# Performance work log

Hardware: AMD Instinct MI355X
Metric: run time of the kernel (lower is better)

Reference implementation:

```python
import jax, jax.numpy as jnp
import numpy as np

V, D, H, T, S = 50000, 256, 512, 16, 8192
H2 = H // 2
START, END = 0, 1
NEG = -10000.0


def setup_inputs() -> dict:
    key = jax.random.key(0)
    ks = jax.random.split(key, 16)

    def rn(k, shape, scale=0.1):
        return jax.random.normal(k, shape, dtype=jnp.float32) * scale

    sentence = jax.random.randint(ks[0], (S,), 0, V)
    emb = rn(ks[1], (V, D), 1.0)
    w_ih_f = rn(ks[2], (4 * H2, D)); w_hh_f = rn(ks[3], (4 * H2, H2))
    b_f = rn(ks[4], (4 * H2,))  # b_ih + b_hh fused
    w_ih_b = rn(ks[5], (4 * H2, D)); w_hh_b = rn(ks[6], (4 * H2, H2))
    b_b = rn(ks[7], (4 * H2,))
    h0_f = rn(ks[8], (H2,), 1.0); c0_f = rn(ks[9], (H2,), 1.0)
    h0_b = rn(ks[10], (H2,), 1.0); c0_b = rn(ks[11], (H2,), 1.0)
    w_out = rn(ks[12], (T, H)); b_out = rn(ks[13], (T,))
    trans = jax.random.normal(ks[14], (T, T), dtype=jnp.float32)
    # transition[START, :] = -10000 ; transition[:, END] = -10000
    trans = trans.at[START, :].set(NEG).at[:, END].set(NEG)
    return {"sentence": sentence, "emb": emb,
            "w_ih_f": w_ih_f, "w_hh_f": w_hh_f, "b_f": b_f,
            "w_ih_b": w_ih_b, "w_hh_b": w_hh_b, "b_b": b_b,
            "h0_f": h0_f, "c0_f": c0_f, "h0_b": h0_b, "c0_b": c0_b,
            "w_out": w_out, "b_out": b_out, "trans": trans}


def _lstm(pre, w_hh, h0, c0):
    # pre: [S, 4*H2] precomputed input projections (x @ W_ih^T + b)
    def step(carry, pre_t):
        h, c = carry
        g = pre_t + w_hh @ h
        i, f, gg, o = jnp.split(g, 4)  # torch gate order: i, f, g, o
        i = jax.nn.sigmoid(i); f = jax.nn.sigmoid(f)
        gg = jnp.tanh(gg); o = jax.nn.sigmoid(o)
        c = f * c + i * gg
        h = o * jnp.tanh(c)
        return (h, c), h
    _, hs = jax.lax.scan(step, (h0, c0), pre)
    return hs  # [S, H2]


def reference(sentence, emb, w_ih_f, w_hh_f, b_f, w_ih_b, w_hh_b, b_b,
              h0_f, c0_f, h0_b, c0_b, w_out, b_out, trans):
    x = emb[sentence]                               # [S, D]
    pre_f = x @ w_ih_f.T + b_f                      # [S, 4*H2]
    pre_b = x[::-1] @ w_ih_b.T + b_b                # reverse direction
    hs_f = _lstm(pre_f, w_hh_f, h0_f, c0_f)         # [S, H2]
    hs_b = _lstm(pre_b, w_hh_b, h0_b, c0_b)[::-1]   # [S, H2]
    feats = jnp.concatenate([hs_f, hs_b], axis=-1) @ w_out.T + b_out  # [S, T]

    # Viterbi (max-plus DP), vectorized over the tag dimension.
    init = jnp.full((T,), NEG, dtype=feats.dtype).at[START].set(0.0)

    def vit_step(score, emit_t):
        cand = score[None, :] + trans               # [T_next, T_prev]
        best = jnp.argmax(cand, axis=1)             # backpointers [T]
        score = jnp.max(cand, axis=1) + emit_t
        return score, best

    last, back = jax.lax.scan(vit_step, init, feats)  # back: [S, T] int
    final = last + trans[END]                       # [T]
    best_last = jnp.argmax(final)
    path_score = final[best_last]

    # Backtrack: path[S-1] = best_last, path[t-1] = back[t][path[t]]
    def back_step(tag, bp_t):
        return bp_t[tag], tag
    _, path = jax.lax.scan(back_step, best_last, back, reverse=True)
    return path_score, path
```

## Files before the change

### kernel.cpp

```cpp
#include <hip/hip_runtime.h>
#include <math.h>

#define SLEN 8192
#define DIM  256
#define H2N  256
#define G4   1024
#define NTAG 16
#define NEGV (-10000.0f)

#define OFF_PRE_F   0
#define OFF_PRE_B   (SLEN*G4)
#define OFF_HS_F    (2*SLEN*G4)
#define OFF_HS_B    (2*SLEN*G4 + SLEN*H2N)
#define OFF_FEATS   (2*SLEN*G4 + 2*SLEN*H2N)
#define OFF_MBOX    (OFF_FEATS + SLEN*NTAG)
#define WS_NEEDED   ((size_t)(OFF_MBOX + 1024) * 4)

typedef unsigned int u32x4 __attribute__((ext_vector_type(4)));

__global__ __launch_bounds__(256) void gemm_pre(
    const int* __restrict__ sent, const float* __restrict__ emb,
    const float* __restrict__ wf, const float* __restrict__ bf,
    const float* __restrict__ wb, const float* __restrict__ bb,
    float* __restrict__ pre_f, float* __restrict__ pre_b)
{
    const int dir = blockIdx.z;
    const float* w    = dir ? wb : wf;
    const float* bias = dir ? bb : bf;
    float* out        = dir ? pre_b : pre_f;
    const int m0 = blockIdx.x * 64, n0 = blockIdx.y * 64;

    __shared__ float As[16][68];
    __shared__ float Bs[16][68];
    __shared__ int   sidx[64];

    const int tid = threadIdx.x;
    const int tx = tid & 15, ty = tid >> 4;

    if (tid < 64) {
        int m = m0 + tid;
        int pos = dir ? (SLEN - 1 - m) : m;
        sidx[tid] = sent[pos];
    }
    __syncthreads();

    float acc[4][4];
#pragma unroll
    for (int i = 0; i < 4; i++)
#pragma unroll
        for (int j = 0; j < 4; j++) acc[i][j] = 0.f;

    const int lr = tid >> 2, lc = (tid & 3) * 4;

    for (int k0 = 0; k0 < DIM; k0 += 16) {
        float4 av = *(const float4*)(emb + (size_t)sidx[lr] * DIM + k0 + lc);
        float4 bv = *(const float4*)(w + (size_t)(n0 + lr) * DIM + k0 + lc);
        As[lc+0][lr] = av.x; As[lc+1][lr] = av.y; As[lc+2][lr] = av.z; As[lc+3][lr] = av.w;
        Bs[lc+0][lr] = bv.x; Bs[lc+1][lr] = bv.y; Bs[lc+2][lr] = bv.z; Bs[lc+3][lr] = bv.w;
        __syncthreads();
#pragma unroll
        for (int k = 0; k < 16; k++) {
            float4 a4 = *(const float4*)&As[k][ty * 4];
            float4 b4 = *(const float4*)&Bs[k][tx * 4];
            float a[4] = {a4.x, a4.y, a4.z, a4.w};
            float b[4] = {b4.x, b4.y, b4.z, b4.w};
#pragma unroll
            for (int i = 0; i < 4; i++)
#pragma unroll
                for (int j = 0; j < 4; j++) acc[i][j] += a[i] * b[j];
        }
        __syncthreads();
    }

    float4 b4 = *(const float4*)(bias + n0 + tx*4);
#pragma unroll
    for (int i = 0; i < 4; i++) {
        float4 v;
        v.x = acc[i][0] + b4.x; v.y = acc[i][1] + b4.y;
        v.z = acc[i][2] + b4.z; v.w = acc[i][3] + b4.w;
        *(float4*)(out + (size_t)(m0 + ty*4 + i) * G4 + n0 + tx*4) = v;
    }
}

__device__ __forceinline__ float fast_sigmoid(float x) {
    return 1.f / (1.f + __expf(-x));
}
__device__ __forceinline__ float fast_tanh(float x) {
    float xc = fminf(fmaxf(x, -15.f), 15.f);
    float e = __expf(2.f * xc);
    return (e - 1.f) / (e + 1.f);
}

__global__ __launch_bounds__(64) void lstm_kernel(
    const float* __restrict__ pre_f, const float* __restrict__ pre_b,
    const float* __restrict__ whh_f, const float* __restrict__ whh_b,
    const float* __restrict__ h0_f, const float* __restrict__ c0_f,
    const float* __restrict__ h0_b, const float* __restrict__ c0_b,
    float* __restrict__ hs_f, float* __restrict__ hs_b,
    unsigned* __restrict__ mbox)
{
    if ((blockIdx.x & 7) > 1) return;
    const int d  = blockIdx.x & 1;
    const int cb = blockIdx.x >> 3;
    const int cell0 = cb * 8;

    const float* pre = d ? pre_b : pre_f;
    const float* whh = d ? whh_b : whh_f;
    const float* h0  = d ? h0_b : h0_f;
    const float* c0  = d ? c0_b : c0_f;
    float* hs        = d ? hs_b : hs_f;

    const int l = threadIdx.x;
    const int r = l >> 1;
    const int half = l & 1;
    const int g = r >> 3, cl = r & 7;
    const int grow = g * 256 + cell0 + cl;

    __shared__ __align__(16) float4 w_pack4[32 * 64];
    __shared__ __align__(16) float  h_lds[256];

    {
        const float4* src = (const float4*)(whh + (size_t)grow * H2N + half * 128);
#pragma unroll
        for (int j = 0; j < 32; j++) w_pack4[j * 64 + l] = src[j];
    }
    ((float4*)h_lds)[l] = ((const float4*)h0)[l];
    float c = (l < 8) ? c0[cell0 + l] : 0.f;
    __syncthreads();

    const float* pre_base = pre + grow;
    float pre_cur = (half == 0) ? pre_base[0] : 0.f;
    const int ai = l & 7;
    unsigned* mb_dir = mbox + d * 512;

    for (int t = 0; t < SLEN; t++) {
        float pre_next = (half == 0 && t < SLEN - 1) ? pre_base[(size_t)(t + 1) * G4] : 0.f;
        const unsigned etag = (((unsigned)t >> 1) & 1u) ^ 1u;
        unsigned* mb = mb_dir + (t & 1) * 256;

        float a0 = pre_cur, a1 = 0.f, a2 = 0.f, a3 = 0.f;
        const float4* hrow4 = (const float4*)(h_lds + half * 128);
#pragma unroll
        for (int j = 0; j < 32; j++) {
            float4 wv = w_pack4[j * 64 + l];
            float4 hv = hrow4[j];
            a0 += wv.x * hv.x; a1 += wv.y * hv.y;
            a2 += wv.z * hv.z; a3 += wv.w * hv.w;
        }
        float sum = (a0 + a1) + (a2 + a3);
        sum += __shfl_xor(sum, 1, 64);

        float s_i = __shfl(sum, 2 * ai, 64);
        float s_f = __shfl(sum, 16 + 2 * ai, 64);
        float s_g = __shfl(sum, 32 + 2 * ai, 64);
        float s_o = __shfl(sum, 48 + 2 * ai, 64);

        if (l < 8) {
            float i_ = fast_sigmoid(s_i);
            float f_ = fast_sigmoid(s_f);
            float g_ = fast_tanh(s_g);
            float o_ = fast_sigmoid(s_o);
            c = f_ * c + i_ * g_;
            float h = o_ * fast_tanh(c);
            unsigned hm = (__float_as_uint(h) & ~1u) | etag;
            __hip_atomic_store(mb + cell0 + l, hm,
                               __ATOMIC_RELAXED, __HIP_MEMORY_SCOPE_AGENT);
            __builtin_nontemporal_store(hm, (unsigned*)hs + (size_t)t * H2N + cell0 + l);
        }

        const unsigned* ms4 = mb + 4 * l;
        u32x4 v;
        int spin = 0;
        for (;;) {
            asm volatile("global_load_dwordx4 %0, %1, off sc0 sc1\n\t"
                         "s_waitcnt vmcnt(0)"
                         : "=v"(v) : "v"(ms4) : "memory");
            if (!(((v.x ^ etag) | (v.y ^ etag) | (v.z ^ etag) | (v.w ^ etag)) & 1u))
                break;
            if (++spin >= 300000) break;
            __builtin_amdgcn_s_sleep(1);
        }

        float4 hv4;
        hv4.x = __uint_as_float(v.x); hv4.y = __uint_as_float(v.y);
        hv4.z = __uint_as_float(v.z); hv4.w = __uint_as_float(v.w);
        *(float4*)(h_lds + 4 * l) = hv4;
        __syncthreads();
        pre_cur = pre_next;
    }
}

__global__ __launch_bounds__(256) void feats_kernel(
    const float* __restrict__ hs_f, const float* __restrict__ hs_b,
    const float* __restrict__ w_out, const float* __restrict__ b_out,
    float* __restrict__ feats)
{
    const int rs0 = blockIdx.x * 16;
    const int tid = threadIdx.x;
    const int r = tid >> 4, cc = tid & 15;

    __shared__ float Hs[16][516];
    for (int i = tid; i < 16 * 256; i += 256) {
        int rr = i >> 8, k = i & 255;
        Hs[rr][k]       = hs_f[(size_t)(rs0 + rr) * H2N + k];
        Hs[rr][256 + k] = hs_b[(size_t)(SLEN - 1 - (rs0 + rr)) * H2N + k];
    }
    __syncthreads();

    float acc = 0.f;
    const float* wr = w_out + (size_t)cc * 512;
    const float* hrow = Hs[r];
#pragma unroll 4
    for (int kq = 0; kq < 128; kq++) {
        float4 hv = *(const float4*)(hrow + 4 * kq);
        float4 wv = *(const float4*)(wr + 4 * kq);
        acc += hv.x * wv.x; acc += hv.y * wv.y;
        acc += hv.z * wv.z; acc += hv.w * wv.w;
    }
    feats[(size_t)(rs0 + r) * NTAG + cc] = acc + b_out[cc];
}

__global__ __launch_bounds__(64) void viterbi_kernel(
    const float* __restrict__ feats, const float* __restrict__ trans,
    float* __restrict__ out)
{
    __shared__ unsigned char back_s[SLEN * 8];

    const int lane = threadIdx.x;
    const int nx = lane >> 2, pc = lane & 3;

    float tr[4];
#pragma unroll
    for (int j = 0; j < 4; j++) tr[j] = trans[nx * NTAG + pc * 4 + j];

    float sc = (nx == 0) ? 0.f : NEGV;
    float fe = feats[nx];

    for (int t = 0; t < SLEN; t++) {
        float fe_next = (t < SLEN - 1) ? feats[(size_t)(t + 1) * NTAG + nx] : 0.f;

        float bv; int bi;
#pragma unroll
        for (int j = 0; j < 4; j++) {
            float s = __shfl(sc, 4 * (pc * 4 + j), 64);
            float cand = s + tr[j];
            if (j == 0) { bv = cand; bi = pc * 4; }
            else if (cand > bv) { bv = cand; bi = pc * 4 + j; }
        }
#pragma unroll
        for (int off = 1; off < 4; off <<= 1) {
            float ov = __shfl_xor(bv, off, 64);
            int   oi = __shfl_xor(bi, off, 64);
            if (ov > bv || (ov == bv && oi < bi)) { bv = ov; bi = oi; }
        }
        int bi_part = __shfl(bi, (nx | 1) * 4, 64);
        if (pc == 0 && (nx & 1) == 0)
            back_s[t * 8 + (nx >> 1)] = (unsigned char)((bi & 15) | (bi_part << 4));
        sc = bv + fe;
        fe = fe_next;
    }

    float bestv = 0.f; int besti = 0;
#pragma unroll
    for (int j = 0; j < NTAG; j++) {
        float sj = __shfl(sc, 4 * j, 64);
        float fj = sj + trans[1 * NTAG + j];
        if (j == 0) { bestv = fj; besti = 0; }
        else if (fj > bestv) { bestv = fj; besti = j; }
    }
    __syncthreads();

    if (lane == 0) {
        out[0] = bestv;
        int cur = besti;
        for (int t = SLEN - 1; t >= 1; t--) {
            out[1 + t] = (float)cur;
            unsigned char byte = back_s[t * 8 + (cur >> 1)];
            cur = (cur & 1) ? (byte >> 4) : (byte & 15);
        }
        out[1] = (float)cur;
    }
}

extern "C" void kernel_launch(void* const* d_in, const int* in_sizes, int n_in,
                              void* d_out, int out_size, void* d_ws, size_t ws_size,
                              hipStream_t stream) {
    const int*   sent   = (const int*)d_in[0];
    const float* emb    = (const float*)d_in[1];
    const float* w_ih_f = (const float*)d_in[2];
    const float* w_hh_f = (const float*)d_in[3];
    const float* b_f    = (const float*)d_in[4];
    const float* w_ih_b = (const float*)d_in[5];
    const float* w_hh_b = (const float*)d_in[6];
    const float* b_b    = (const float*)d_in[7];
    const float* h0_f   = (const float*)d_in[8];
    const float* c0_f   = (const float*)d_in[9];
    const float* h0_b   = (const float*)d_in[10];
    const float* c0_b   = (const float*)d_in[11];
    const float* w_out  = (const float*)d_in[12];
    const float* b_out  = (const float*)d_in[13];
    const float* trans  = (const float*)d_in[14];
    float* out = (float*)d_out;

    if (ws_size < WS_NEEDED) return;

    float* ws = (float*)d_ws;
    float* pre_f = ws + OFF_PRE_F;
    float* pre_b = ws + OFF_PRE_B;
    float* hs_f  = ws + OFF_HS_F;
    float* hs_b  = ws + OFF_HS_B;
    float* feats = ws + OFF_FEATS;
    unsigned* mbox = (unsigned*)(ws + OFF_MBOX);

    gemm_pre<<<dim3(128, 16, 2), 256, 0, stream>>>(sent, emb, w_ih_f, b_f, w_ih_b, b_b, pre_f, pre_b);
    lstm_kernel<<<256, 64, 0, stream>>>(pre_f, pre_b, w_hh_f, w_hh_b,
                                        h0_f, c0_f, h0_b, c0_b, hs_f, hs_b, mbox);
    feats_kernel<<<512, 256, 0, stream>>>(hs_f, hs_b, w_out, b_out, feats);
    viterbi_kernel<<<1, 64, 0, stream>>>(feats, trans, out);
}
```

Measured before the change: 22.16 ms.

## Repartition LSTM recurrence into 16 blocks of 256 threads with LDS gate reduction

The recurrent LSTM kernel moves from 64 active single-wave blocks (8 cells each) to 16 blocks of four waves, each block owning 32 cells per direction. Gate sums are gathered through shared memory instead of cross-lane shuffles, and only wave 0 does the global mailbox exchange and spin-wait. Fewer blocks take part in the per-step cross-block handshake, which is meant to cut synchronisation latency on each of the serial timesteps. In exchange it adds an extra __syncthreads per step, keeps part of the weights in registers because of the LDS size limit, and drops the s_sleep inside the spin loop.

```diff
diff --git a/kernel.cpp b/kernel.cpp
--- a/kernel.cpp
+++ b/kernel.cpp
@@ -91,7 +91,7 @@
     return (e - 1.f) / (e + 1.f);
 }
 
-__global__ __launch_bounds__(64) void lstm_kernel(
+__global__ __launch_bounds__(256) void lstm_kernel(
     const float* __restrict__ pre_f, const float* __restrict__ pre_b,
     const float* __restrict__ whh_f, const float* __restrict__ whh_b,
     const float* __restrict__ h0_f, const float* __restrict__ c0_f,
@@ -99,10 +99,10 @@
     float* __restrict__ hs_f, float* __restrict__ hs_b,
     unsigned* __restrict__ mbox)
 {
-    if ((blockIdx.x & 7) > 1) return;
-    const int d  = blockIdx.x & 1;
-    const int cb = blockIdx.x >> 3;
-    const int cell0 = cb * 8;
+    const int b  = blockIdx.x;
+    const int d  = b & 1;
+    const int cb = b >> 1;
+    const int cell0 = cb * 32;
 
     const float* pre = d ? pre_b : pre_f;
     const float* whh = d ? whh_b : whh_f;
@@ -110,27 +110,31 @@
     const float* c0  = d ? c0_b : c0_f;
     float* hs        = d ? hs_b : hs_f;
 
-    const int l = threadIdx.x;
-    const int r = l >> 1;
-    const int half = l & 1;
-    const int g = r >> 3, cl = r & 7;
-    const int grow = g * 256 + cell0 + cl;
-
-    __shared__ __align__(16) float4 w_pack4[32 * 64];
+    const int tid  = threadIdx.x;
+    const int lane = tid & 63;
+    const int wv   = tid >> 6;
+    const int r    = tid >> 1;
+    const int half = tid & 1;
+    const int cl   = r & 31;
+    const int grow = wv * 256 + cell0 + cl;
+
+    __shared__ __align__(16) float4 w4[30 * 256];
     __shared__ __align__(16) float  h_lds[256];
-
+    __shared__ float gsum[128];
+
+    float4 wr30, wr31;
     {
         const float4* src = (const float4*)(whh + (size_t)grow * H2N + half * 128);
 #pragma unroll
-        for (int j = 0; j < 32; j++) w_pack4[j * 64 + l] = src[j];
-    }
-    ((float4*)h_lds)[l] = ((const float4*)h0)[l];
-    float c = (l < 8) ? c0[cell0 + l] : 0.f;
+        for (int j = 0; j < 30; j++) w4[j * 256 + tid] = src[j];
+        wr30 = src[30]; wr31 = src[31];
+    }
+    if (tid < 64) ((float4*)h_lds)[tid] = ((const float4*)h0)[tid];
+    float c = (wv == 0 && lane < 32) ? c0[cell0 + lane] : 0.f;
     __syncthreads();
 
     const float* pre_base = pre + grow;
     float pre_cur = (half == 0) ? pre_base[0] : 0.f;
-    const int ai = l & 7;
     unsigned* mb_dir = mbox + d * 512;
 
     for (int t = 0; t < SLEN; t++) {
@@ -139,52 +143,68 @@
         unsigned* mb = mb_dir + (t & 1) * 256;
 
         float a0 = pre_cur, a1 = 0.f, a2 = 0.f, a3 = 0.f;
-        const float4* hrow4 = (const float4*)(h_lds + half * 128);
-#pragma unroll
-        for (int j = 0; j < 32; j++) {
-            float4 wv = w_pack4[j * 64 + l];
-            float4 hv = hrow4[j];
-            a0 += wv.x * hv.x; a1 += wv.y * hv.y;
-            a2 += wv.z * hv.z; a3 += wv.w * hv.w;
+        const float4* hr4 = (const float4*)(h_lds + half * 128);
+#pragma unroll
+        for (int j = 0; j < 30; j++) {
+            float4 wvv = w4[j * 256 + tid];
+            float4 hv  = hr4[j];
+            a0 += wvv.x * hv.x; a1 += wvv.y * hv.y;
+            a2 += wvv.z * hv.z; a3 += wvv.w * hv.w;
+        }
+        {
+            float4 hv = hr4[30];
+            a0 += wr30.x * hv.x; a1 += wr30.y * hv.y;
+            a2 += wr30.z * hv.z; a3 += wr30.w * hv.w;
+        }
+        {
+            float4 hv = hr4[31];
+            a0 += wr31.x * hv.x; a1 += wr31.y * hv.y;
+            a2 += wr31.z * hv.z; a3 += wr31.w * hv.w;
         }
         float sum = (a0 + a1) + (a2 + a3);
         sum += __shfl_xor(sum, 1, 64);
 
-        float s_i = __shfl(sum, 2 * ai, 64);
-        float s_f = __shfl(sum, 16 + 2 * ai, 64);
-        float s_g = __shfl(sum, 32 + 2 * ai, 64);
-        float s_o = __shfl(sum, 48 + 2 * ai, 64);
-
-        if (l < 8) {
-            float i_ = fast_sigmoid(s_i);
-            float f_ = fast_sigmoid(s_f);
-            float g_ = fast_tanh(s_g);
-            float o_ = fast_sigmoid(s_o);
-            c = f_ * c + i_ * g_;
-            float h = o_ * fast_tanh(c);
-            unsigned hm = (__float_as_uint(h) & ~1u) | etag;
-            __hip_atomic_store(mb + cell0 + l, hm,
-                               __ATOMIC_RELAXED, __HIP_MEMORY_SCOPE_AGENT);
-            __builtin_nontemporal_store(hm, (unsigned*)hs + (size_t)t * H2N + cell0 + l);
-        }
-
-        const unsigned* ms4 = mb + 4 * l;
-        u32x4 v;
-        int spin = 0;
-        for (;;) {
-            asm volatile("global_load_dwordx4 %0, %1, off sc0 sc1\n\t"
-                         "s_waitcnt vmcnt(0)"
-                         : "=v"(v) : "v"(ms4) : "memory");
-            if (!(((v.x ^ etag) | (v.y ^ etag) | (v.z ^ etag) | (v.w ^ etag)) & 1u))
-                break;
-            if (++spin >= 300000) break;
-            __builtin_amdgcn_s_sleep(1);
-        }
-
-        float4 hv4;
-        hv4.x = __uint_as_float(v.x); hv4.y = __uint_as_float(v.y);
-        hv4.z = __uint_as_float(v.z); hv4.w = __uint_as_float(v.w);
-        *(float4*)(h_lds + 4 * l) = hv4;
+        if (!half) gsum[wv * 32 + cl] = sum;
+        __syncthreads();
+
+        if (wv == 0) {
+            unsigned hm = 0;
+            if (lane < 32) {
+                float s_i = gsum[lane];
+                float s_f = gsum[32 + lane];
+                float s_g = gsum[64 + lane];
+                float s_o = gsum[96 + lane];
+                float i_ = fast_sigmoid(s_i);
+                float f_ = fast_sigmoid(s_f);
+                float g_ = fast_tanh(s_g);
+                float o_ = fast_sigmoid(s_o);
+                c = f_ * c + i_ * g_;
+                float h = o_ * fast_tanh(c);
+                hm = (__float_as_uint(h) & ~1u) | etag;
+                __hip_atomic_store(mb + cell0 + lane, hm,
+                                   __ATOMIC_RELAXED, __HIP_MEMORY_SCOPE_AGENT);
+            }
+
+            const unsigned* ms4 = mb + 4 * lane;
+            u32x4 v;
+            int spin = 0;
+            for (;;) {
+                asm volatile("global_load_dwordx4 %0, %1, off sc0 sc1\n\t"
+                             "s_waitcnt vmcnt(0)"
+                             : "=v"(v) : "v"(ms4) : "memory");
+                if (!(((v.x ^ etag) | (v.y ^ etag) | (v.z ^ etag) | (v.w ^ etag)) & 1u))
+                    break;
+                if (++spin >= 300000) break;
+            }
+            float4 hv4;
+            hv4.x = __uint_as_float(v.x); hv4.y = __uint_as_float(v.y);
+            hv4.z = __uint_as_float(v.z); hv4.w = __uint_as_float(v.w);
+            *(float4*)(h_lds + 4 * lane) = hv4;
+
+            if (lane < 32)
+                __builtin_nontemporal_store(hm,
+                    (unsigned*)hs + (size_t)t * H2N + cell0 + lane);
+        }
         __syncthreads();
         pre_cur = pre_next;
     }
@@ -313,7 +333,7 @@
     unsigned* mbox = (unsigned*)(ws + OFF_MBOX);
 
     gemm_pre<<<dim3(128, 16, 2), 256, 0, stream>>>(sent, emb, w_ih_f, b_f, w_ih_b, b_b, pre_f, pre_b);
-    lstm_kernel<<<256, 64, 0, stream>>>(pre_f, pre_b, w_hh_f, w_hh_b,
+    lstm_kernel<<<16, 256, 0, stream>>>(pre_f, pre_b, w_hh_f, w_hh_b,
                                         h0_f, c0_f, h0_b, c0_b, hs_f, hs_b, mbox);
     feats_kernel<<<512, 256, 0, stream>>>(hs_f, hs_b, w_out, b_out, feats);
     viterbi_kernel<<<1, 64, 0, stream>>>(feats, trans, out);
```

Result: faster. 21.31 ms (-3.8%).

## Run each LSTM direction in one 512-thread block with fp16 register-resident weights

Applied to the files above, without the earlier changes.

Replaces the multi-block LSTM recurrence, which exchanged hidden states through a global-memory mailbox with spin-waiting, with one workgroup per direction. The recurrent weights are packed to fp16: three quarters stay in registers and the rest in LDS. Dot products use fdot2 with DPP reductions, and synchronisation becomes block barriers. This removes cross-block global sync latency per timestep, at the cost of fp16 precision in weights and hidden state and of using only two CUs.

```diff
diff --git a/kernel.cpp b/kernel.cpp
--- a/kernel.cpp
+++ b/kernel.cpp
@@ -13,10 +13,39 @@
 #define OFF_HS_F    (2*SLEN*G4)
 #define OFF_HS_B    (2*SLEN*G4 + SLEN*H2N)
 #define OFF_FEATS   (2*SLEN*G4 + 2*SLEN*H2N)
-#define OFF_MBOX    (OFF_FEATS + SLEN*NTAG)
-#define WS_NEEDED   ((size_t)(OFF_MBOX + 1024) * 4)
+#define WS_NEEDED   ((size_t)(OFF_FEATS + SLEN*NTAG) * 4)
 
 typedef unsigned int u32x4 __attribute__((ext_vector_type(4)));
+typedef __fp16 h2_t __attribute__((ext_vector_type(2)));
+
+__device__ __forceinline__ unsigned pack2(float x, float y) {
+#if __has_builtin(__builtin_amdgcn_cvt_pkrtz)
+    return __builtin_bit_cast(unsigned, __builtin_amdgcn_cvt_pkrtz(x, y));
+#else
+    union { __fp16 h[2]; unsigned u; } t;
+    t.h[0] = (__fp16)x; t.h[1] = (__fp16)y;
+    return t.u;
+#endif
+}
+
+#if __has_builtin(__builtin_amdgcn_fdot2)
+__device__ __forceinline__ float fdot2(unsigned a, unsigned b, float c) {
+    return __builtin_amdgcn_fdot2(__builtin_bit_cast(h2_t, a),
+                                  __builtin_bit_cast(h2_t, b), c, false);
+}
+#else
+__device__ __forceinline__ float fdot2(unsigned a, unsigned b, float c) {
+    union { unsigned u; __fp16 h[2]; } ua, ub;
+    ua.u = a; ub.u = b;
+    return c + (float)ua.h[0] * (float)ub.h[0] + (float)ua.h[1] * (float)ub.h[1];
+}
+#endif
+
+template <int CTRL>
+__device__ __forceinline__ float dpp_add(float x) {
+    int v = __builtin_amdgcn_update_dpp(0, __float_as_int(x), CTRL, 0xF, 0xF, true);
+    return x + __int_as_float(v);
+}
 
 __global__ __launch_bounds__(256) void gemm_pre(
     const int* __restrict__ sent, const float* __restrict__ emb,
@@ -91,102 +120,138 @@
     return (e - 1.f) / (e + 1.f);
 }
 
-__global__ __launch_bounds__(64) void lstm_kernel(
+__global__ __launch_bounds__(512) void lstm_kernel(
     const float* __restrict__ pre_f, const float* __restrict__ pre_b,
     const float* __restrict__ whh_f, const float* __restrict__ whh_b,
     const float* __restrict__ h0_f, const float* __restrict__ c0_f,
     const float* __restrict__ h0_b, const float* __restrict__ c0_b,
-    float* __restrict__ hs_f, float* __restrict__ hs_b,
-    unsigned* __restrict__ mbox)
+    float* __restrict__ hs_f, float* __restrict__ hs_b)
 {
-    if ((blockIdx.x & 7) > 1) return;
-    const int d  = blockIdx.x & 1;
-    const int cb = blockIdx.x >> 3;
-    const int cell0 = cb * 8;
-
+    const int d = blockIdx.x;
     const float* pre = d ? pre_b : pre_f;
     const float* whh = d ? whh_b : whh_f;
     const float* h0  = d ? h0_b : h0_f;
     const float* c0  = d ? c0_b : c0_f;
     float* hs        = d ? hs_b : hs_f;
 
-    const int l = threadIdx.x;
-    const int r = l >> 1;
-    const int half = l & 1;
-    const int g = r >> 3, cl = r & 7;
-    const int grow = g * 256 + cell0 + cl;
-
-    __shared__ __align__(16) float4 w_pack4[32 * 64];
-    __shared__ __align__(16) float  h_lds[256];
-
-    {
-        const float4* src = (const float4*)(whh + (size_t)grow * H2N + half * 128);
-#pragma unroll
-        for (int j = 0; j < 32; j++) w_pack4[j * 64 + l] = src[j];
-    }
-    ((float4*)h_lds)[l] = ((const float4*)h0)[l];
-    float c = (l < 8) ? c0[cell0 + l] : 0.f;
+    const int tid = threadIdx.x;
+    const int l   = tid & 63;
+    const int w   = tid >> 6;
+    const int kg  = l & 7;
+    const int rl  = l >> 3;
+    const int slot = w * 8 + rl;
+    const int k0 = kg * 32;
+
+    __shared__ __align__(16) u32x4  wlds[16][512];
+    __shared__ __align__(16) __fp16 hbuf[256];
+    __shared__ __align__(16) float  gsum[1024];
+
+    unsigned wreg[12][16];
+#pragma unroll
+    for (int i = 0; i < 16; i++) {
+        const float* wsrc = whh + (size_t)(slot + 64 * i) * H2N + k0;
+        unsigned pk[16];
+#pragma unroll
+        for (int q = 0; q < 8; q++) {
+            float4 v = *(const float4*)(wsrc + 4 * q);
+            pk[2 * q]     = pack2(v.x, v.y);
+            pk[2 * q + 1] = pack2(v.z, v.w);
+        }
+        if (i < 12) {
+#pragma unroll
+            for (int p = 0; p < 16; p++) wreg[i][p] = pk[p];
+        } else {
+#pragma unroll
+            for (int c4 = 0; c4 < 4; c4++) {
+                u32x4 vv;
+                vv.x = pk[4*c4+0]; vv.y = pk[4*c4+1];
+                vv.z = pk[4*c4+2]; vv.w = pk[4*c4+3];
+                wlds[(i - 12) * 4 + c4][tid] = vv;
+            }
+        }
+    }
+
+    float cst = 0.f, prg0 = 0.f, prg1 = 0.f, prg2 = 0.f, prg3 = 0.f;
+    if (tid < 256) {
+        hbuf[tid] = (__fp16)h0[tid];
+        cst  = c0[tid];
+        prg0 = pre[0 * 256 + tid];
+        prg1 = pre[1 * 256 + tid];
+        prg2 = pre[2 * 256 + tid];
+        prg3 = pre[3 * 256 + tid];
+    }
     __syncthreads();
 
-    const float* pre_base = pre + grow;
-    float pre_cur = (half == 0) ? pre_base[0] : 0.f;
-    const int ai = l & 7;
-    unsigned* mb_dir = mbox + d * 512;
-
     for (int t = 0; t < SLEN; t++) {
-        float pre_next = (half == 0 && t < SLEN - 1) ? pre_base[(size_t)(t + 1) * G4] : 0.f;
-        const unsigned etag = (((unsigned)t >> 1) & 1u) ^ 1u;
-        unsigned* mb = mb_dir + (t & 1) * 256;
-
-        float a0 = pre_cur, a1 = 0.f, a2 = 0.f, a3 = 0.f;
-        const float4* hrow4 = (const float4*)(h_lds + half * 128);
-#pragma unroll
-        for (int j = 0; j < 32; j++) {
-            float4 wv = w_pack4[j * 64 + l];
-            float4 hv = hrow4[j];
-            a0 += wv.x * hv.x; a1 += wv.y * hv.y;
-            a2 += wv.z * hv.z; a3 += wv.w * hv.w;
-        }
-        float sum = (a0 + a1) + (a2 + a3);
-        sum += __shfl_xor(sum, 1, 64);
-
-        float s_i = __shfl(sum, 2 * ai, 64);
-        float s_f = __shfl(sum, 16 + 2 * ai, 64);
-        float s_g = __shfl(sum, 32 + 2 * ai, 64);
-        float s_o = __shfl(sum, 48 + 2 * ai, 64);
-
-        if (l < 8) {
+        unsigned hreg[16];
+        {
+            const u32x4* hp = (const u32x4*)((const char*)hbuf + kg * 64);
+#pragma unroll
+            for (int j = 0; j < 4; j++) {
+                u32x4 hv = hp[j];
+                hreg[4*j+0] = hv.x; hreg[4*j+1] = hv.y;
+                hreg[4*j+2] = hv.z; hreg[4*j+3] = hv.w;
+            }
+        }
+
+#pragma unroll
+        for (int b = 0; b < 4; b++) {
+            float sv[4];
+#pragma unroll
+            for (int ii = 0; ii < 4; ii++) {
+                const int i = 4 * b + ii;
+                float a0 = 0.f, a1 = 0.f;
+                if (i < 12) {
+#pragma unroll
+                    for (int p = 0; p < 16; p += 2) {
+                        a0 = fdot2(wreg[i][p],     hreg[p],     a0);
+                        a1 = fdot2(wreg[i][p + 1], hreg[p + 1], a1);
+                    }
+                } else {
+#pragma unroll
+                    for (int c4 = 0; c4 < 4; c4++) {
+                        u32x4 wc = wlds[(i - 12) * 4 + c4][tid];
+                        a0 = fdot2(wc.x, hreg[4*c4+0], a0);
+                        a1 = fdot2(wc.y, hreg[4*c4+1], a1);
+                        a0 = fdot2(wc.z, hreg[4*c4+2], a0);
+                        a1 = fdot2(wc.w, hreg[4*c4+3], a1);
+                    }
+                }
+                float a = a0 + a1;
+                a = dpp_add<0xB1>(a);
+                a = dpp_add<0x4E>(a);
+                a = dpp_add<0x141>(a);
+                sv[ii] = a;
+            }
+            if (kg == 0) {
+                float4 o; o.x = sv[0]; o.y = sv[1]; o.z = sv[2]; o.w = sv[3];
+                *(float4*)(gsum + slot * 16 + ((b ^ (slot & 3)) << 2)) = o;
+            }
+        }
+        __syncthreads();
+
+        if (tid < 256) {
+            const int cc = tid, sl = cc & 63, chi = cc >> 6;
+            float s_i = gsum[sl * 16 + ((0 ^ (sl & 3)) << 2) + chi] + prg0;
+            float s_f = gsum[sl * 16 + ((1 ^ (sl & 3)) << 2) + chi] + prg1;
+            float s_g = gsum[sl * 16 + ((2 ^ (sl & 3)) << 2) + chi] + prg2;
+            float s_o = gsum[sl * 16 + ((3 ^ (sl & 3)) << 2) + chi] + prg3;
             float i_ = fast_sigmoid(s_i);
             float f_ = fast_sigmoid(s_f);
             float g_ = fast_tanh(s_g);
             float o_ = fast_sigmoid(s_o);
-            c = f_ * c + i_ * g_;
-            float h = o_ * fast_tanh(c);
-            unsigned hm = (__float_as_uint(h) & ~1u) | etag;
-            __hip_atomic_store(mb + cell0 + l, hm,
-                               __ATOMIC_RELAXED, __HIP_MEMORY_SCOPE_AGENT);
-            __builtin_nontemporal_store(hm, (unsigned*)hs + (size_t)t * H2N + cell0 + l);
-        }
-
-        const unsigned* ms4 = mb + 4 * l;
-        u32x4 v;
-        int spin = 0;
-        for (;;) {
-            asm volatile("global_load_dwordx4 %0, %1, off sc0 sc1\n\t"
-                         "s_waitcnt vmcnt(0)"
-                         : "=v"(v) : "v"(ms4) : "memory");
-            if (!(((v.x ^ etag) | (v.y ^ etag) | (v.z ^ etag) | (v.w ^ etag)) & 1u))
-                break;
-            if (++spin >= 300000) break;
-            __builtin_amdgcn_s_sleep(1);
-        }
-
-        float4 hv4;
-        hv4.x = __uint_as_float(v.x); hv4.y = __uint_as_float(v.y);
-        hv4.z = __uint_as_float(v.z); hv4.w = __uint_as_float(v.w);
-        *(float4*)(h_lds + 4 * l) = hv4;
+            cst = f_ * cst + i_ * g_;
+            float h = o_ * fast_tanh(cst);
+            __fp16 hh = (__fp16)h;
+            hbuf[cc] = hh;
+            __builtin_nontemporal_store((float)hh, hs + (size_t)t * H2N + cc);
+            if (t < SLEN - 1) {
+                const float* pn = pre + (size_t)(t + 1) * G4 + cc;
+                prg0 = pn[0];   prg1 = pn[256];
+                prg2 = pn[512]; prg3 = pn[768];
+            }
+        }
         __syncthreads();
-        pre_cur = pre_next;
     }
 }
 
@@ -310,11 +375,10 @@
     float* hs_f  = ws + OFF_HS_F;
     float* hs_b  = ws + OFF_HS_B;
     float* feats = ws + OFF_FEATS;
-    unsigned* mbox = (unsigned*)(ws + OFF_MBOX);
 
     gemm_pre<<<dim3(128, 16, 2), 256, 0, stream>>>(sent, emb, w_ih_f, b_f, w_ih_b, b_b, pre_f, pre_b);
-    lstm_kernel<<<256, 64, 0, stream>>>(pre_f, pre_b, w_hh_f, w_hh_b,
-                                        h0_f, c0_f, h0_b, c0_b, hs_f, hs_b, mbox);
+    lstm_kernel<<<2, 512, 0, stream>>>(pre_f, pre_b, w_hh_f, w_hh_b,
+                                       h0_f, c0_f, h0_b, c0_b, hs_f, hs_b);
     feats_kernel<<<512, 256, 0, stream>>>(hs_f, hs_b, w_out, b_out, feats);
     viterbi_kernel<<<1, 64, 0, stream>>>(feats, trans, out);
 }
```

After: 19.81 ms. -10.6%, faster.
